# Optimization experiments

Measured on AMD Instinct MI355X. Metric: run time of the kernel, lower is better.

## Reference

```python
import jax, jax.numpy as jnp
import numpy as np

N_NODES = 50000
N_EDGES = 800000
HIDDEN = 128
POS = 16
LAYERS = 8
HEADS = 8
HEAD_DIM = HIDDEN // HEADS
OUT = 10
N_GRAPHS = 128


def setup_inputs() -> dict:
    key = jax.random.key(0)
    ks = jax.random.split(key, 16)
    s = 1.0 / np.sqrt(HIDDEN)
    inp = {
        "X": jax.random.normal(ks[0], (N_NODES, HIDDEN), jnp.float32),
        "pos_enc": jax.random.normal(ks[1], (N_NODES, POS), jnp.float32),
        "edge_row": jnp.sort(jax.random.randint(ks[2], (N_EDGES,), 0, N_NODES, jnp.int32)),
        "edge_col": jax.random.randint(ks[3], (N_EDGES,), 0, N_NODES, jnp.int32),
        "graph_ids": jnp.sort(jax.random.randint(ks[4], (N_NODES,), 0, N_GRAPHS, jnp.int32)),
        # parameters
        "Wpos": jax.random.normal(ks[5], (POS, HIDDEN), jnp.float32) / np.sqrt(POS),
        "bpos": jnp.zeros((HIDDEN,), jnp.float32),
        "Wq": jax.random.normal(ks[6], (LAYERS, HIDDEN, HIDDEN), jnp.float32) * s,
        "bq": jnp.zeros((LAYERS, HIDDEN), jnp.float32),
        "Wk": jax.random.normal(ks[7], (LAYERS, HIDDEN, HIDDEN), jnp.float32) * s,
        "bk": jnp.zeros((LAYERS, HIDDEN), jnp.float32),
        "Wv": jax.random.normal(ks[8], (LAYERS, HIDDEN, HIDDEN), jnp.float32) * s,
        "bv": jnp.zeros((LAYERS, HIDDEN), jnp.float32),
        "Wpred": jax.random.normal(ks[9], (HIDDEN, OUT), jnp.float32) * s,
        "bpred": jnp.zeros((OUT,), jnp.float32),
    }
    return inp


def _sparse_mha(h, row, col, Wq, bq, Wk, bk, Wv, bv):
    # one SparseMHA layer: per-head SDDMM scores on edges, edge softmax per
    # destination (row of sparse A), SpMM aggregation.
    N = h.shape[0]
    scale = HEAD_DIM ** -0.5
    q = ((h @ Wq + bq).reshape(N, HEADS, HEAD_DIM)) * scale
    k = (h @ Wk + bk).reshape(N, HEADS, HEAD_DIM)
    v = (h @ Wv + bv).reshape(N, HEADS, HEAD_DIM)
    score = jnp.einsum("ehd,ehd->eh", q[row], k[col])            # [E,H]
    m = jax.ops.segment_max(score, row, num_segments=N)           # [N,H]
    ex = jnp.exp(score - m[row])
    denom = jax.ops.segment_sum(ex, row, num_segments=N)          # [N,H]
    attn = ex / denom[row]                                        # [E,H]
    out = jax.ops.segment_sum(attn[:, :, None] * v[col], row, num_segments=N)
    return out.reshape(N, HIDDEN)


def reference(X, pos_enc, edge_row, edge_col, graph_ids,
              Wpos, bpos, Wq, bq, Wk, bk, Wv, bv, Wpred, bpred):
    h = pos_enc @ Wpos + bpos                                     # [N, HIDDEN]

    def step(h, p):
        wq, bq_, wk, bk_, wv, bv_ = p
        return _sparse_mha(h, edge_row, edge_col, wq, bq_, wk, bk_, wv, bv_), None

    h, _ = jax.lax.scan(step, h, (Wq, bq, Wk, bk, Wv, bv))
    pooled = jax.ops.segment_sum(h, graph_ids, num_segments=N_GRAPHS)  # [G, HIDDEN]
    return pooled @ Wpred + bpred                                  # [G, OUT]
```

## Files before the change

### kernel.cpp

```cpp
#include <hip/hip_runtime.h>
#include <hip/hip_bf16.h>
#include <math.h>

#define N_NODES 50000
#define N_PADR  50048
#define N_EDGES 800000
#define HIDDEN  128
#define POS_DIM 16
#define LAYERS  8
#define HEADS   8
#define HEAD_DIM 16
#define OUT_DIM 10
#define N_GRAPHS 128

using f32x4 = __attribute__((ext_vector_type(4))) float;
using half8 = __attribute__((ext_vector_type(8))) _Float16;
typedef _Float16 h2 __attribute__((ext_vector_type(2)));

#if defined(__has_builtin)
#if __has_builtin(__builtin_amdgcn_fdot2)
#define HAVE_FDOT2 1
#endif
#endif

__device__ __forceinline__ unsigned packh2(float a, float b) {
    union { h2 h; unsigned u; } t;
    t.h = (h2){(_Float16)a, (_Float16)b};
    return t.u;
}
__device__ __forceinline__ float dot8(uint4 k, const unsigned* q, float s) {
#if defined(HAVE_FDOT2)
    union { unsigned u; h2 h; } a, b;
    a.u = k.x; b.u = q[0]; s = __builtin_amdgcn_fdot2(a.h, b.h, s, false);
    a.u = k.y; b.u = q[1]; s = __builtin_amdgcn_fdot2(a.h, b.h, s, false);
    a.u = k.z; b.u = q[2]; s = __builtin_amdgcn_fdot2(a.h, b.h, s, false);
    a.u = k.w; b.u = q[3]; s = __builtin_amdgcn_fdot2(a.h, b.h, s, false);
    return s;
#else
    union { unsigned u; h2 h; } a, b;
#pragma unroll
    for (int j = 0; j < 4; ++j) {
        a.u = (&k.x)[j]; b.u = q[j];
        s += (float)a.h[0] * (float)b.h[0] + (float)a.h[1] * (float)b.h[1];
    }
    return s;
#endif
}

__global__ void k_row_ptr(const int* __restrict__ row, int* __restrict__ row_ptr) {
    int e = blockIdx.x * blockDim.x + threadIdx.x;
    if (e >= N_EDGES) return;
    int cur  = row[e];
    int prev = (e == 0) ? -1 : row[e - 1];
    for (int r = prev + 1; r <= cur; ++r) row_ptr[r] = e;
    if (e == N_EDGES - 1) {
        for (int r = cur + 1; r <= N_NODES; ++r) row_ptr[r] = N_EDGES;
    }
}

__global__ __launch_bounds__(256) void k_wprep(const float* __restrict__ Wq,
                                               const float* __restrict__ Wk,
                                               const float* __restrict__ Wv,
                                               unsigned short* __restrict__ Wt) {
    __shared__ float sT[32][33];
    const int l3 = blockIdx.x >> 4, tile = blockIdx.x & 15;
    const int layer = l3 / 3, mat = l3 % 3;
    const float* src = (mat == 0 ? Wq : mat == 1 ? Wk : Wv) + (size_t)layer * HIDDEN * HIDDEN;
    const float scl = (mat == 0) ? 0.25f : 1.0f;
    unsigned short* dh = Wt + (size_t)l3 * HIDDEN * HIDDEN;
    const int k0 = (tile >> 2) * 32, n0 = (tile & 3) * 32;
    const int tx = threadIdx.x & 31, ty = threadIdx.x >> 5;
#pragma unroll
    for (int i = 0; i < 4; ++i)
        sT[ty + i * 8][tx] = src[(size_t)(k0 + ty + i * 8) * HIDDEN + n0 + tx];
    __syncthreads();
#pragma unroll
    for (int i = 0; i < 4; ++i) {
        const int nr = ty + i * 8;
        union { h2 h; unsigned u; } t;
        t.h = (h2){(_Float16)(sT[tx][nr] * scl), (_Float16)0.f};
        dh[(size_t)(n0 + nr) * HIDDEN + k0 + tx] = (unsigned short)(t.u & 0xffffu);
    }
}

__global__ __launch_bounds__(256) void k_pos(const float* __restrict__ pos,
                                             const float* __restrict__ Wpos,
                                             const float* __restrict__ bpos,
                                             unsigned short* __restrict__ h) {
    __shared__ float sW[POS_DIM][HIDDEN];
    __shared__ float sb[HIDDEN];
    int t = threadIdx.x;
    for (int i = t; i < POS_DIM * HIDDEN; i += 256) sW[i / HIDDEN][i % HIDDEN] = Wpos[i];
    if (t < HIDDEN) sb[t] = bpos[t];
    __syncthreads();
    int n = blockIdx.x * 2 + (t >> 7);
    int j = t & 127;
    if (n >= N_NODES) return;
    float acc = sb[j];
#pragma unroll
    for (int q = 0; q < POS_DIM; ++q) acc += pos[n * POS_DIM + q] * sW[q][j];
    union { h2 h; unsigned u; } v;
    v.h = (h2){(_Float16)acc, (_Float16)0.f};
    h[(size_t)n * HIDDEN + j] = (unsigned short)(v.u & 0xffffu);
}

__global__ __launch_bounds__(256) void k_qkv(const unsigned short* __restrict__ h,
                                             const unsigned short* __restrict__ Wt,
                                             const float* __restrict__ bq,
                                             const float* __restrict__ bk,
                                             const float* __restrict__ bv,
                                             unsigned* __restrict__ Qh,
                                             unsigned short* __restrict__ KV,
                                             int layer) {
    __shared__ unsigned char sA[64 * 256];

    const int t = threadIdx.x;
    const int w = t >> 6, lane = t & 63;
    const int c = lane >> 4, r = lane & 15;
    const int m0 = blockIdx.x * 64;
    const int mat = blockIdx.y;

    {
        const char* src = (const char*)h + (size_t)m0 * 256;
#pragma unroll
        for (int i = 0; i < 4; ++i) {
            const int s   = i * 256 + t;
            const int row = s >> 4;
            const int ch  = s & 15;
            const char* g = src + row * 256 + ((ch ^ (row & 15)) << 4);
            char* l = (char*)&sA[(i * 256 + w * 64) << 4];
            __builtin_amdgcn_global_load_lds(
                (const __attribute__((address_space(1))) unsigned int*)g,
                (__attribute__((address_space(3))) unsigned int*)l, 16, 0, 0);
        }
    }

    const unsigned short* wt = Wt + (size_t)(layer * 3 + mat) * (HIDDEN * HIDDEN);
    const int nbase = w * 2;
    half8 B[2][4];
#pragma unroll
    for (int nbp = 0; nbp < 2; ++nbp)
#pragma unroll
        for (int kc = 0; kc < 4; ++kc)
            B[nbp][kc] = *(const half8*)&wt[(size_t)((nbase + nbp) * 16 + r) * HIDDEN + kc * 32 + c * 8];

    __syncthreads();

    f32x4 acc[4][2];
#pragma unroll
    for (int mb = 0; mb < 4; ++mb)
#pragma unroll
        for (int nbp = 0; nbp < 2; ++nbp)
            acc[mb][nbp] = (f32x4){0.f, 0.f, 0.f, 0.f};

#pragma unroll
    for (int mb = 0; mb < 4; ++mb) {
        const int abase = (mb * 16 + r) * 256;
        half8 a[4];
#pragma unroll
        for (int kc = 0; kc < 4; ++kc)
            a[kc] = *(const half8*)&sA[abase + ((((kc << 2) + c) ^ r) << 4)];
#pragma unroll
        for (int nbp = 0; nbp < 2; ++nbp)
#pragma unroll
            for (int kc = 0; kc < 4; ++kc)
                acc[mb][nbp] = __builtin_amdgcn_mfma_f32_16x16x32_f16(B[nbp][kc], a[kc], acc[mb][nbp], 0, 0, 0);
    }

    const float* bias = (mat == 0 ? bq : mat == 1 ? bk : bv) + layer * HIDDEN;
#pragma unroll
    for (int mb = 0; mb < 4; ++mb) {
        const size_t m = m0 + mb * 16 + r;
#pragma unroll
        for (int nbp = 0; nbp < 2; ++nbp) {
            const int n0 = (nbase + nbp) * 16 + c * 4;
            float4 b4 = *(const float4*)&bias[n0];
            float v0, v1, v2, v3;
            if (mat == 0) {
                v0 = acc[mb][nbp][0] + b4.x * 0.25f;
                v1 = acc[mb][nbp][1] + b4.y * 0.25f;
                v2 = acc[mb][nbp][2] + b4.z * 0.25f;
                v3 = acc[mb][nbp][3] + b4.w * 0.25f;
            } else {
                v0 = acc[mb][nbp][0] + b4.x;
                v1 = acc[mb][nbp][1] + b4.y;
                v2 = acc[mb][nbp][2] + b4.z;
                v3 = acc[mb][nbp][3] + b4.w;
            }
            uint2 o = make_uint2(packh2(v0, v1), packh2(v2, v3));
            if (mat == 0) {
                *(uint2*)&Qh[m * 64 + (n0 >> 1)] = o;
            } else {
                unsigned short* dst = KV + m * 256 + (mat == 2 ? 128 : 0) + n0;
                *(uint2*)dst = o;
            }
        }
    }
}

__global__ __launch_bounds__(256) void k_attn(const unsigned* __restrict__ Qh,
                                              const unsigned short* __restrict__ KV,
                                              const int* __restrict__ col,
                                              const int* __restrict__ row_ptr,
                                              unsigned short* __restrict__ hout) {
    int wid  = (blockIdx.x * blockDim.x + threadIdx.x) >> 6;
    int lane = threadIdx.x & 63;
    if (wid >= N_NODES) return;
    const int g  = lane >> 3;
    const int lg = lane & 7;
    const int d0 = lg * 16;
    const int start = row_ptr[wid];
    const int end   = row_ptr[wid + 1];

    unsigned q2[8];
    {
        uint4 qa = *(const uint4*)&Qh[(size_t)wid * 64 + lg * 8];
        uint4 qb = *(const uint4*)&Qh[(size_t)wid * 64 + lg * 8 + 4];
        q2[0] = qa.x; q2[1] = qa.y; q2[2] = qa.z; q2[3] = qa.w;
        q2[4] = qb.x; q2[5] = qb.y; q2[6] = qb.z; q2[7] = qb.w;
    }

    float dsum = 0.f;
    float acc[16];
#pragma unroll
    for (int i = 0; i < 16; ++i) acc[i] = 0.f;

    int e = start + g;
    int c = (e < end) ? col[e] : -1;
    uint4 kA, kB, vA, vB;
    if (c >= 0) {
        const uint4* kp = (const uint4*)(KV + (size_t)c * 256 + d0);
        const uint4* vp = (const uint4*)(KV + (size_t)c * 256 + 128 + d0);
        kA = kp[0]; kB = kp[1]; vA = vp[0]; vB = vp[1];
    }
    while (c >= 0) {
        int en = e + 8;
        int cn = (en < end) ? col[en] : -1;
        uint4 nkA, nkB, nvA, nvB;
        if (cn >= 0) {
            const uint4* kp = (const uint4*)(KV + (size_t)cn * 256 + d0);
            const uint4* vp = (const uint4*)(KV + (size_t)cn * 256 + 128 + d0);
            nkA = kp[0]; nkB = kp[1]; nvA = vp[0]; nvB = vp[1];
        }
        float s = dot8(kA, q2, 0.f);
        s = dot8(kB, q2 + 4, s);
        float p = __expf(s);
        dsum += p;
        union { unsigned u; h2 h; } tv;
#pragma unroll
        for (int j = 0; j < 4; ++j) {
            tv.u = (&vA.x)[j];
            acc[2 * j]     += p * (float)tv.h[0];
            acc[2 * j + 1] += p * (float)tv.h[1];
        }
#pragma unroll
        for (int j = 0; j < 4; ++j) {
            tv.u = (&vB.x)[j];
            acc[8 + 2 * j]     += p * (float)tv.h[0];
            acc[8 + 2 * j + 1] += p * (float)tv.h[1];
        }
        e = en; c = cn;
        kA = nkA; kB = nkB; vA = nvA; vB = nvB;
    }
#pragma unroll
    for (int off = 8; off < 64; off <<= 1) {
        dsum += __shfl_xor(dsum, off);
#pragma unroll
        for (int i = 0; i < 16; ++i) acc[i] += __shfl_xor(acc[i], off);
    }
    if (g == 0) {
        float inv = (end > start) ? 1.f / fmaxf(dsum, 1e-30f) : 0.f;
        unsigned hw[8];
#pragma unroll
        for (int j = 0; j < 8; ++j)
            hw[j] = packh2(acc[2 * j] * inv, acc[2 * j + 1] * inv);
        uint4* ph = (uint4*)(hout + (size_t)wid * HIDDEN + d0);
        ph[0] = make_uint4(hw[0], hw[1], hw[2], hw[3]);
        ph[1] = make_uint4(hw[4], hw[5], hw[6], hw[7]);
    }
}

__global__ __launch_bounds__(256) void k_pool(const unsigned short* __restrict__ h,
                                              const int* __restrict__ gid,
                                              float* __restrict__ pooled) {
    const int ch   = threadIdx.x & 127;
    const int half = threadIdx.x >> 7;
    const int n0   = blockIdx.x * 128 + half * 64;
    float run = 0.f;
    int   rg  = -1;
    for (int i = 0; i < 64; ++i) {
        int n = n0 + i;
        if (n >= N_NODES) break;
        int g = gid[n];
        if (g != rg) {
            if (rg >= 0) atomicAdd(&pooled[rg * HIDDEN + ch], run);
            rg = g; run = 0.f;
        }
        union { unsigned u; h2 hh; } v;
        v.u = (unsigned)h[(size_t)n * HIDDEN + ch];
        run += (float)v.hh[0];
    }
    if (rg >= 0) atomicAdd(&pooled[rg * HIDDEN + ch], run);
}

__global__ void k_pred(const float* __restrict__ pooled, const float* __restrict__ Wp,
                       const float* __restrict__ bp, float* __restrict__ out) {
    int idx = blockIdx.x * blockDim.x + threadIdx.x;
    if (idx >= N_GRAPHS * OUT_DIM) return;
    int g = idx / OUT_DIM, o = idx % OUT_DIM;
    float acc = bp[o];
#pragma unroll 4
    for (int j = 0; j < HIDDEN; ++j) acc += pooled[g * HIDDEN + j] * Wp[j * OUT_DIM + o];
    out[idx] = acc;
}

extern "C" void kernel_launch(void* const* d_in, const int* in_sizes, int n_in,
                              void* d_out, int out_size, void* d_ws, size_t ws_size,
                              hipStream_t stream) {
    const float* pos   = (const float*)d_in[1];
    const int*   erow  = (const int*)d_in[2];
    const int*   ecol  = (const int*)d_in[3];
    const int*   gid   = (const int*)d_in[4];
    const float* Wpos  = (const float*)d_in[5];
    const float* bpos  = (const float*)d_in[6];
    const float* Wq    = (const float*)d_in[7];
    const float* bq    = (const float*)d_in[8];
    const float* Wk    = (const float*)d_in[9];
    const float* bk    = (const float*)d_in[10];
    const float* Wv    = (const float*)d_in[11];
    const float* bv    = (const float*)d_in[12];
    const float* Wpred = (const float*)d_in[13];
    const float* bpred = (const float*)d_in[14];
    float* out = (float*)d_out;

    char* base = (char*)d_ws;
    size_t off = 0;
    auto alloc = [&](size_t bytes) {
        void* r = base + off;
        off += (bytes + 255) & ~(size_t)255;
        return r;
    };
    unsigned short* h    = (unsigned short*)alloc((size_t)N_PADR * HIDDEN * 2);
    unsigned*       Qh   = (unsigned*)alloc((size_t)N_PADR * 64 * 4);
    unsigned short* KVb  = (unsigned short*)alloc((size_t)N_PADR * 256 * 2);
    unsigned short* Wt   = (unsigned short*)alloc((size_t)LAYERS * 3 * HIDDEN * HIDDEN * 2);
    int*   rowp   = (int*)alloc((size_t)(N_NODES + 1) * 4);
    float* pooled = (float*)alloc((size_t)N_GRAPHS * HIDDEN * 4);

    k_row_ptr<<<(N_EDGES + 255) / 256, 256, 0, stream>>>(erow, rowp);
    k_wprep<<<LAYERS * 3 * 16, 256, 0, stream>>>(Wq, Wk, Wv, Wt);
    k_pos<<<N_NODES / 2, 256, 0, stream>>>(pos, Wpos, bpos, h);

    for (int l = 0; l < LAYERS; ++l) {
        dim3 g(N_PADR / 64, 3, 1);
        k_qkv<<<g, 256, 0, stream>>>(h, Wt, bq, bk, bv, Qh, KVb, l);
        k_attn<<<(N_NODES * 64 + 255) / 256, 256, 0, stream>>>(Qh, KVb, ecol, rowp, h);
    }

    hipMemsetAsync(pooled, 0, N_GRAPHS * HIDDEN * 4, stream);
    k_pool<<<(N_NODES + 127) / 128, 256, 0, stream>>>(h, gid, pooled);
    k_pred<<<(N_GRAPHS * OUT_DIM + 255) / 256, 256, 0, stream>>>(pooled, Wpred, bpred, out);
}
```

Measured before the change: 848.0 us.

## Retile QKV GEMM to per-wave 32x32 tiles without LDS; batch pos kernel rows

The QKV projection kernel drops its shared-memory staging of a 64-row A tile. Each wave now independently computes a 32-row by 32-column tile of one of Q/K/V, loading A and B fragments directly from global memory into registers, which removes the LDS copy and the __syncthreads. In exchange, A rows are re-read by the four column-block waves and all three matrices rather than shared through LDS, raising global/L2 traffic. The positional-encoding kernel also processes 64 nodes per block instead of 2, cutting block count and the repeated loading of Wpos into shared memory.

```diff
diff --git a/kernel.cpp b/kernel.cpp
--- a/kernel.cpp
+++ b/kernel.cpp
@@ -93,15 +93,18 @@
     for (int i = t; i < POS_DIM * HIDDEN; i += 256) sW[i / HIDDEN][i % HIDDEN] = Wpos[i];
     if (t < HIDDEN) sb[t] = bpos[t];
     __syncthreads();
-    int n = blockIdx.x * 2 + (t >> 7);
-    int j = t & 127;
-    if (n >= N_NODES) return;
-    float acc = sb[j];
-#pragma unroll
-    for (int q = 0; q < POS_DIM; ++q) acc += pos[n * POS_DIM + q] * sW[q][j];
-    union { h2 h; unsigned u; } v;
-    v.h = (h2){(_Float16)acc, (_Float16)0.f};
-    h[(size_t)n * HIDDEN + j] = (unsigned short)(v.u & 0xffffu);
+    const int j = t & 127, half = t >> 7;
+#pragma unroll 4
+    for (int i = 0; i < 32; ++i) {
+        int n = blockIdx.x * 64 + half * 32 + i;
+        if (n >= N_NODES) break;
+        float acc = sb[j];
+#pragma unroll
+        for (int q = 0; q < POS_DIM; ++q) acc += pos[n * POS_DIM + q] * sW[q][j];
+        union { h2 hh; unsigned u; } v;
+        v.hh = (h2){(_Float16)acc, (_Float16)0.f};
+        h[(size_t)n * HIDDEN + j] = (unsigned short)(v.u & 0xffffu);
+    }
 }
 
 __global__ __launch_bounds__(256) void k_qkv(const unsigned short* __restrict__ h,
@@ -112,68 +115,50 @@
                                              unsigned* __restrict__ Qh,
                                              unsigned short* __restrict__ KV,
                                              int layer) {
-    __shared__ unsigned char sA[64 * 256];
-
     const int t = threadIdx.x;
-    const int w = t >> 6, lane = t & 63;
+    const int lane = t & 63;
     const int c = lane >> 4, r = lane & 15;
-    const int m0 = blockIdx.x * 64;
-    const int mat = blockIdx.y;
-
-    {
-        const char* src = (const char*)h + (size_t)m0 * 256;
-#pragma unroll
-        for (int i = 0; i < 4; ++i) {
-            const int s   = i * 256 + t;
-            const int row = s >> 4;
-            const int ch  = s & 15;
-            const char* g = src + row * 256 + ((ch ^ (row & 15)) << 4);
-            char* l = (char*)&sA[(i * 256 + w * 64) << 4];
-            __builtin_amdgcn_global_load_lds(
-                (const __attribute__((address_space(1))) unsigned int*)g,
-                (__attribute__((address_space(3))) unsigned int*)l, 16, 0, 0);
-        }
-    }
+    const int W = blockIdx.x * 4 + (t >> 6);
+    const int tr  = W / 12;
+    const int rem = W - tr * 12;
+    const int cb  = rem / 3;
+    const int mat = rem - cb * 3;
+    const int m0 = tr * 32;
 
     const unsigned short* wt = Wt + (size_t)(layer * 3 + mat) * (HIDDEN * HIDDEN);
-    const int nbase = w * 2;
-    half8 B[2][4];
-#pragma unroll
-    for (int nbp = 0; nbp < 2; ++nbp)
-#pragma unroll
-        for (int kc = 0; kc < 4; ++kc)
-            B[nbp][kc] = *(const half8*)&wt[(size_t)((nbase + nbp) * 16 + r) * HIDDEN + kc * 32 + c * 8];
-
-    __syncthreads();
-
-    f32x4 acc[4][2];
-#pragma unroll
-    for (int mb = 0; mb < 4; ++mb)
+    const int koff = c * 8;
+
+    half8 a[2][4], B[2][4];
+#pragma unroll
+    for (int kc = 0; kc < 4; ++kc) {
+        a[0][kc] = *(const half8*)&h[(size_t)(m0 + r) * HIDDEN + kc * 32 + koff];
+        a[1][kc] = *(const half8*)&h[(size_t)(m0 + 16 + r) * HIDDEN + kc * 32 + koff];
+        B[0][kc] = *(const half8*)&wt[(size_t)((cb * 2 + 0) * 16 + r) * HIDDEN + kc * 32 + koff];
+        B[1][kc] = *(const half8*)&wt[(size_t)((cb * 2 + 1) * 16 + r) * HIDDEN + kc * 32 + koff];
+    }
+
+    f32x4 acc[2][2];
+#pragma unroll
+    for (int mb = 0; mb < 2; ++mb)
 #pragma unroll
         for (int nbp = 0; nbp < 2; ++nbp)
             acc[mb][nbp] = (f32x4){0.f, 0.f, 0.f, 0.f};
 
 #pragma unroll
-    for (int mb = 0; mb < 4; ++mb) {
-        const int abase = (mb * 16 + r) * 256;
-        half8 a[4];
-#pragma unroll
-        for (int kc = 0; kc < 4; ++kc)
-            a[kc] = *(const half8*)&sA[abase + ((((kc << 2) + c) ^ r) << 4)];
+    for (int mb = 0; mb < 2; ++mb)
 #pragma unroll
         for (int nbp = 0; nbp < 2; ++nbp)
 #pragma unroll
             for (int kc = 0; kc < 4; ++kc)
-                acc[mb][nbp] = __builtin_amdgcn_mfma_f32_16x16x32_f16(B[nbp][kc], a[kc], acc[mb][nbp], 0, 0, 0);
-    }
+                acc[mb][nbp] = __builtin_amdgcn_mfma_f32_16x16x32_f16(B[nbp][kc], a[mb][kc], acc[mb][nbp], 0, 0, 0);
 
     const float* bias = (mat == 0 ? bq : mat == 1 ? bk : bv) + layer * HIDDEN;
 #pragma unroll
-    for (int mb = 0; mb < 4; ++mb) {
+    for (int mb = 0; mb < 2; ++mb) {
         const size_t m = m0 + mb * 16 + r;
 #pragma unroll
         for (int nbp = 0; nbp < 2; ++nbp) {
-            const int n0 = (nbase + nbp) * 16 + c * 4;
+            const int n0 = cb * 32 + nbp * 16 + c * 4;
             float4 b4 = *(const float4*)&bias[n0];
             float v0, v1, v2, v3;
             if (mat == 0) {
@@ -349,11 +334,11 @@
 
     k_row_ptr<<<(N_EDGES + 255) / 256, 256, 0, stream>>>(erow, rowp);
     k_wprep<<<LAYERS * 3 * 16, 256, 0, stream>>>(Wq, Wk, Wv, Wt);
-    k_pos<<<N_NODES / 2, 256, 0, stream>>>(pos, Wpos, bpos, h);
-
+    k_pos<<<(N_NODES + 63) / 64, 256, 0, stream>>>(pos, Wpos, bpos, h);
+
+    const int qkv_blocks = (N_PADR / 32) * 12 / 4;
     for (int l = 0; l < LAYERS; ++l) {
-        dim3 g(N_PADR / 64, 3, 1);
-        k_qkv<<<g, 256, 0, stream>>>(h, Wt, bq, bk, bv, Qh, KVb, l);
+        k_qkv<<<qkv_blocks, 256, 0, stream>>>(h, Wt, bq, bk, bv, Qh, KVb, l);
         k_attn<<<(N_NODES * 64 + 255) / 256, 256, 0, stream>>>(Qh, KVb, ecol, rowp, h);
     }
 
```

New measurement: 960.4 us. 13.2% more time.
